# Kernel tuning notes

Measured on AMD Instinct MI355X. Metric: run time of the kernel, lower is better.

## Reference

```python
import jax, jax.numpy as jnp
import numpy as np

def mish(x):
    return x * jnp.tanh(jax.nn.softplus(x))

def setup_inputs() -> dict:
    ANT, RF, DS, G, B = 64, 8, 8, 16, 4096
    BB_DIM = 2 * RF * DS      # 128
    RF_DIM = 2 * ANT * RF     # 1024
    key = jax.random.key(0)
    ks = jax.random.split(key, 10)
    def lin(kw, kb, i, o):
        lim = 1.0 / np.sqrt(i)
        W = jax.random.uniform(kw, (o, i), jnp.float32, -lim, lim)
        b = jax.random.uniform(kb, (o,), jnp.float32, -lim, lim)
        return W, b
    W_rfbb, b_rfbb = lin(ks[0], ks[1], RF_DIM, BB_DIM)
    W_rfrf, b_rfrf = lin(ks[2], ks[3], RF_DIM, RF_DIM)
    W_bbrf, b_bbrf = lin(ks[4], ks[5], BB_DIM, RF_DIM)
    W_bbbb, b_bbbb = lin(ks[6], ks[7], BB_DIM, BB_DIM)
    BB_feature = jax.random.normal(ks[8], (B, G, BB_DIM), jnp.float32)
    RF_feature = jax.random.normal(ks[9], (B, RF_DIM), jnp.float32)
    return {
        "BB_feature": BB_feature, "RF_feature": RF_feature,
        "W_rfbb": W_rfbb, "b_rfbb": b_rfbb,
        "W_rfrf": W_rfrf, "b_rfrf": b_rfrf,
        "W_bbrf": W_bbrf, "b_bbrf": b_bbrf,
        "W_bbbb": W_bbbb, "b_bbbb": b_bbbb,
    }

def reference(BB_feature, RF_feature, W_rfbb, b_rfbb, W_rfrf, b_rfrf, W_bbrf, b_bbrf, W_bbbb, b_bbbb):
    # mean over subcarrier-group dim
    BB_mean = jnp.mean(BB_feature, axis=-2)                      # [B, BB_DIM]
    RF_to_RF = mish(RF_feature @ W_rfrf.T + b_rfrf)              # [B, RF_DIM]
    RF_to_BB = mish(RF_feature @ W_rfbb.T + b_rfbb)              # [B, BB_DIM]
    BB_to_RF = mish(BB_mean @ W_bbrf.T + b_bbrf)                 # [B, RF_DIM]
    BB_to_BB = mish(jnp.einsum('bgi,oi->bgo', BB_feature, W_bbbb) + b_bbbb)  # [B, G, BB_DIM]
    new_RF = RF_to_RF + BB_to_RF
    new_BB = BB_to_BB + RF_to_BB[:, None, :]
    return (new_BB, new_RF)
```

## Files before the change

### kernel.cpp

```cpp
#include <hip/hip_runtime.h>
#include <hip/hip_bf16.h>

typedef __attribute__((ext_vector_type(8))) short short8;
typedef __attribute__((ext_vector_type(4))) short short4v;
typedef __attribute__((ext_vector_type(4))) float floatx4;

#define BDIM 128
#define RDIM 1024
#define NB   4096
#define NG   16

__device__ __forceinline__ float mishf(float x) {
    float e = __expf(x);
    float t = e * (e + 2.0f);
    float r = x * (t / (t + 2.0f));
    return x > 20.0f ? x : r;
}

__device__ __forceinline__ short8 cvt8v(float4 f0, float4 f1) {
    union { __hip_bfloat162 h; unsigned u; } c0, c1, c2, c3;
    c0.h = __float22bfloat162_rn(make_float2(f0.x, f0.y));
    c1.h = __float22bfloat162_rn(make_float2(f0.z, f0.w));
    c2.h = __float22bfloat162_rn(make_float2(f1.x, f1.y));
    c3.h = __float22bfloat162_rn(make_float2(f1.z, f1.w));
    union { short8 s; unsigned u[4]; } r;
    r.u[0] = c0.u; r.u[1] = c1.u; r.u[2] = c2.u; r.u[3] = c3.u;
    return r.s;
}

__device__ __forceinline__ short4v cvt4v(float4 f) {
    union { __hip_bfloat162 h; unsigned u; } c0, c1;
    c0.h = __float22bfloat162_rn(make_float2(f.x, f.y));
    c1.h = __float22bfloat162_rn(make_float2(f.z, f.w));
    union { short4v s; unsigned u[2]; } r;
    r.u[0] = c0.u; r.u[1] = c1.u;
    return r.s;
}

__device__ __forceinline__ void gld16(const void* g, void* l) {
    __builtin_amdgcn_global_load_lds(
        (const __attribute__((address_space(1))) unsigned int*)g,
        (__attribute__((address_space(3))) unsigned int*)l, 16, 0, 0);
}

#define MFMA(a, b, c) __builtin_amdgcn_mfma_f32_16x16x32_bf16(a, b, c, 0, 0, 0)

#define RF_N     4194304u
#define C1       4194304u
#define C2       5242880u
#define C3       5373952u
#define C4       5505024u
#define CT       5521408u

__global__ void __launch_bounds__(256) k_prep(
    const float* __restrict__ bb, const float* __restrict__ rf,
    const float* __restrict__ Wrfrf, const float* __restrict__ Wrfbb,
    const float* __restrict__ Wbbrf, const float* __restrict__ Wbbbb,
    short* __restrict__ bb_b, short* __restrict__ mean_b, short* __restrict__ rf_b,
    short* __restrict__ wrfrf_b, short* __restrict__ wrfbb_b,
    short* __restrict__ wbbrf_b, short* __restrict__ wbbbb_b)
{
    int bid = blockIdx.x;
    int tid = threadIdx.x;
    if (bid < 512) {
        int b = bid * 8 + (tid >> 5);
        int d = (tid & 31) * 4;
        const float4* p = (const float4*)(bb + (size_t)b * (NG * BDIM) + d);
        short* ob = bb_b + (size_t)b * (NG * BDIM) + d;
        float4 s = {0.f, 0.f, 0.f, 0.f};
        #pragma unroll
        for (int g = 0; g < NG; ++g) {
            float4 v = p[g * (BDIM / 4)];
            s.x += v.x; s.y += v.y; s.z += v.z; s.w += v.w;
            *(short4v*)(ob + g * BDIM) = cvt4v(v);
        }
        s.x *= 0.0625f; s.y *= 0.0625f; s.z *= 0.0625f; s.w *= 0.0625f;
        *(short4v*)(mean_b + (size_t)b * BDIM + d) = cvt4v(s);
    } else {
        size_t t = (size_t)(bid - 512) * 256 + tid;
        for (size_t base = t * 8; base < CT; base += (size_t)512 * 256 * 8) {
            const float* s; short* dst; size_t off;
            if (base < C1)      { s = rf;    dst = rf_b;    off = base; }
            else if (base < C2) { s = Wrfrf; dst = wrfrf_b; off = base - C1; }
            else if (base < C3) { s = Wrfbb; dst = wrfbb_b; off = base - C2; }
            else if (base < C4) { s = Wbbrf; dst = wbbrf_b; off = base - C3; }
            else                { s = Wbbbb; dst = wbbbb_b; off = base - C4; }
            float4 f0 = ((const float4*)(s + off))[0];
            float4 f1 = ((const float4*)(s + off))[1];
            *(short8*)(dst + off) = cvt8v(f0, f1);
        }
    }
}

__global__ void __launch_bounds__(256) k_newrf(
    const short* __restrict__ rfb,
    const short* __restrict__ meanb,
    const short* __restrict__ wrfrfb,
    const float* __restrict__ brfrf,
    const short* __restrict__ wbbrfb,
    const float* __restrict__ bbbrf,
    const short* __restrict__ wrfbbb,
    const float* __restrict__ brfbb,
    float* __restrict__ out,
    float* __restrict__ rf2bb)
{
    __shared__ alignas(16) short As[2][128 * 64];
    __shared__ alignas(16) short Bs[2][64 * 64];
    __shared__ alignas(16) short Ws2[2][16 * 64];
    int tid = threadIdx.x;
    int wave = tid >> 6, lane = tid & 63;
    int r = lane & 15, quad = lane >> 4;
    int wm = (wave & 1) * 64, wn = (wave >> 1) * 32;
    int mt = blockIdx.x >> 4, nt = blockIdx.x & 15;
    int m0 = mt * 128, n0 = nt * 64;
    bool doP = (nt < 8);

    int srow = lane >> 3;
    int scol = ((lane & 7) ^ srow) * 8;

    const short* aB = rfb    + (size_t)(m0 + wave * 32 + srow) * RDIM + scol;
    const short* bB = wrfrfb + (size_t)(n0 + wave * 16 + srow) * RDIM + scol;
    const short* wB = wrfbbb + (size_t)(nt * 16 + srow) * RDIM + scol;

    floatx4 acc1[4][2], acc2[4][2], acc3[4];
    #pragma unroll
    for (int mi = 0; mi < 4; ++mi) {
        acc1[mi][0] = floatx4{0.f,0.f,0.f,0.f}; acc1[mi][1] = acc1[mi][0];
        acc2[mi][0] = acc1[mi][0]; acc2[mi][1] = acc1[mi][0];
        acc3[mi] = acc1[mi][0];
    }

    auto stage1 = [&](int buf, int k) {
        #pragma unroll
        for (int j = 0; j < 4; ++j)
            gld16(aB + (size_t)j * 8 * RDIM + k, &As[buf][(wave * 32 + j * 8) * 64]);
        #pragma unroll
        for (int j = 0; j < 2; ++j)
            gld16(bB + (size_t)j * 8 * RDIM + k, &Bs[buf][(wave * 16 + j * 8) * 64]);
        if (doP && wave == 0) {
            #pragma unroll
            for (int j = 0; j < 2; ++j)
                gld16(wB + (size_t)j * 8 * RDIM + k, &Ws2[buf][j * 8 * 64]);
        }
    };

    stage1(0, 0);
    __syncthreads();

    for (int it = 0; it < 16; ++it) {
        int buf = it & 1;
        if (it < 15) stage1(buf ^ 1, (it + 1) * 64);
        const short* Ac = As[buf];
        const short* Bc = Bs[buf];
        const short* Wc = Ws2[buf];
        #pragma unroll
        for (int kk = 0; kk < 2; ++kk) {
            int sw = (((kk << 2) + quad) ^ (r & 7)) << 3;
            short8 af[4];
            #pragma unroll
            for (int mi = 0; mi < 4; ++mi)
                af[mi] = *(const short8*)&Ac[(wm + mi * 16 + r) * 64 + sw];
            short8 bf0 = *(const short8*)&Bc[(wn + r) * 64 + sw];
            short8 bf1 = *(const short8*)&Bc[(wn + 16 + r) * 64 + sw];
            #pragma unroll
            for (int mi = 0; mi < 4; ++mi) {
                acc1[mi][0] = MFMA(af[mi], bf0, acc1[mi][0]);
                acc1[mi][1] = MFMA(af[mi], bf1, acc1[mi][1]);
            }
            if (doP && (wave & 2) == 0) {
                short8 b2 = *(const short8*)&Wc[r * 64 + sw];
                #pragma unroll
                for (int mi = 0; mi < 4; ++mi) acc3[mi] = MFMA(af[mi], b2, acc3[mi]);
            }
        }
        __syncthreads();
    }

    const short* a2B = meanb  + (size_t)(m0 + wave * 32 + srow) * BDIM + scol;
    const short* b2B = wbbrfb + (size_t)(n0 + wave * 16 + srow) * BDIM + scol;
    auto stage2 = [&](int buf, int k) {
        #pragma unroll
        for (int j = 0; j < 4; ++j)
            gld16(a2B + (size_t)j * 8 * BDIM + k, &As[buf][(wave * 32 + j * 8) * 64]);
        #pragma unroll
        for (int j = 0; j < 2; ++j)
            gld16(b2B + (size_t)j * 8 * BDIM + k, &Bs[buf][(wave * 16 + j * 8) * 64]);
    };
    stage2(0, 0);
    __syncthreads();
    for (int it = 0; it < 2; ++it) {
        int buf = it & 1;
        if (it < 1) stage2(1, 64);
        const short* Ac = As[buf];
        const short* Bc = Bs[buf];
        #pragma unroll
        for (int kk = 0; kk < 2; ++kk) {
            int sw = (((kk << 2) + quad) ^ (r & 7)) << 3;
            short8 af[4];
            #pragma unroll
            for (int mi = 0; mi < 4; ++mi)
                af[mi] = *(const short8*)&Ac[(wm + mi * 16 + r) * 64 + sw];
            short8 bf0 = *(const short8*)&Bc[(wn + r) * 64 + sw];
            short8 bf1 = *(const short8*)&Bc[(wn + 16 + r) * 64 + sw];
            #pragma unroll
            for (int mi = 0; mi < 4; ++mi) {
                acc2[mi][0] = MFMA(af[mi], bf0, acc2[mi][0]);
                acc2[mi][1] = MFMA(af[mi], bf1, acc2[mi][1]);
            }
        }
        __syncthreads();
    }

    #pragma unroll
    for (int nj = 0; nj < 2; ++nj) {
        int col = n0 + wn + nj * 16 + r;
        float b1 = brfrf[col];
        float b2 = bbbrf[col];
        #pragma unroll
        for (int mi = 0; mi < 4; ++mi) {
            #pragma unroll
            for (int g = 0; g < 4; ++g) {
                int row = m0 + wm + mi * 16 + quad * 4 + g;
                out[(size_t)row * RDIM + col] =
                    mishf(acc1[mi][nj][g] + b1) + mishf(acc2[mi][nj][g] + b2);
            }
        }
    }
    if (doP && (wave & 2) == 0) {
        int col = nt * 16 + r;
        float bs = brfbb[col];
        #pragma unroll
        for (int mi = 0; mi < 4; ++mi) {
            #pragma unroll
            for (int g = 0; g < 4; ++g) {
                int row = m0 + wm + mi * 16 + quad * 4 + g;
                rf2bb[(size_t)row * BDIM + col] = mishf(acc3[mi][g] + bs);
            }
        }
    }
}

__global__ void __launch_bounds__(256) k_newbb(
    const short* __restrict__ bbb,
    const short* __restrict__ wb,
    const float* __restrict__ bias,
    const float* __restrict__ rf2bb,
    float* __restrict__ out)
{
    __shared__ alignas(16) short At[128 * 128];
    __shared__ alignas(16) short Wt[128 * 128];
    int tid = threadIdx.x;
    int wave = tid >> 6, lane = tid & 63;
    int r = lane & 15, quad = lane >> 4;
    size_t m0 = (size_t)blockIdx.x * 128;

    int lrow = lane >> 4;
    int lslot = lane & 15;
    #pragma unroll
    for (int j = 0; j < 8; ++j) {
        int row = wave * 32 + j * 4 + lrow;
        int col = ((lslot ^ (row & 7)) << 3);
        gld16(bbb + (m0 + row) * BDIM + col, &At[(wave * 32 + j * 4) * 128]);
        gld16(wb + (size_t)row * BDIM + col,  &Wt[(wave * 32 + j * 4) * 128]);
    }

    floatx4 acc[2][8];
    #pragma unroll
    for (int i = 0; i < 2; ++i)
        #pragma unroll
        for (int j = 0; j < 8; ++j) acc[i][j] = floatx4{0.f,0.f,0.f,0.f};

    __syncthreads();

    #pragma unroll
    for (int kc = 0; kc < 4; ++kc) {
        int sw = (((kc << 2) + quad) ^ (r & 7)) << 3;
        short8 a0 = *(const short8*)&At[(wave * 32 + r) * 128 + sw];
        short8 a1 = *(const short8*)&At[(wave * 32 + 16 + r) * 128 + sw];
        #pragma unroll
        for (int nj = 0; nj < 8; ++nj) {
            short8 b = *(const short8*)&Wt[(nj * 16 + r) * 128 + sw];
            acc[0][nj] = MFMA(a0, b, acc[0][nj]);
            acc[1][nj] = MFMA(a1, b, acc[1][nj]);
        }
    }

    #pragma unroll
    for (int mi = 0; mi < 2; ++mi) {
        #pragma unroll
        for (int nj = 0; nj < 8; ++nj) {
            int col = nj * 16 + r;
            float bs = bias[col];
            #pragma unroll
            for (int g = 0; g < 4; ++g) {
                size_t row = m0 + wave * 32 + mi * 16 + quad * 4 + g;
                out[row * BDIM + col] = mishf(acc[mi][nj][g] + bs) + rf2bb[(row >> 4) * BDIM + col];
            }
        }
    }
}

extern "C" void kernel_launch(void* const* d_in, const int* in_sizes, int n_in,
                              void* d_out, int out_size, void* d_ws, size_t ws_size,
                              hipStream_t stream) {
    const float* BB    = (const float*)d_in[0];
    const float* RF    = (const float*)d_in[1];
    const float* Wrfbb = (const float*)d_in[2];
    const float* brfbb = (const float*)d_in[3];
    const float* Wrfrf = (const float*)d_in[4];
    const float* brfrf = (const float*)d_in[5];
    const float* Wbbrf = (const float*)d_in[6];
    const float* bbbrf = (const float*)d_in[7];
    const float* Wbbbb = (const float*)d_in[8];
    const float* bbbbb = (const float*)d_in[9];

    float* outBB = (float*)d_out;
    float* outRF = outBB + (size_t)NB * NG * BDIM;

    char* w = (char*)d_ws;
    short* mean_b  = (short*)(w);
    short* rf_b    = (short*)(w + 1048576);
    short* wrfrf_b = (short*)(w + 9437184);
    short* wrfbb_b = (short*)(w + 11534336);
    short* wbbrf_b = (short*)(w + 11796480);
    short* wbbbb_b = (short*)(w + 12058624);
    short* bb_b    = (short*)(w + 12091392);
    float* rf2bb   = (float*)(w + 28868608);

    k_prep <<<1024, 256, 0, stream>>>(BB, RF, Wrfrf, Wrfbb, Wbbrf, Wbbbb,
                                      bb_b, mean_b, rf_b, wrfrf_b, wrfbb_b,
                                      wbbrf_b, wbbbb_b);
    k_newrf<<<512, 256, 0, stream>>>(rf_b, mean_b, wrfrf_b, brfrf, wbbrf_b, bbbrf,
                                     wrfbb_b, brfbb, outRF, rf2bb);
    k_newbb<<<512, 256, 0, stream>>>(bb_b, wbbbb_b, bbbbb, rf2bb, outBB);
}
```

Before: 153.0 us.

## Split RF-to-BB GEMM into separate blocks and use register-staged LDS loads

```diff
diff --git a/kernel.cpp b/kernel.cpp
--- a/kernel.cpp
+++ b/kernel.cpp
@@ -9,6 +9,7 @@
 #define RDIM 1024
 #define NB   4096
 #define NG   16
+#define LDP  66
 
 __device__ __forceinline__ float mishf(float x) {
     float e = __expf(x);
@@ -45,12 +46,12 @@
 
 #define MFMA(a, b, c) __builtin_amdgcn_mfma_f32_16x16x32_bf16(a, b, c, 0, 0, 0)
 
-#define RF_N     4194304u
 #define C1       4194304u
 #define C2       5242880u
 #define C3       5373952u
 #define C4       5505024u
 #define CT       5521408u
+#define FLATB    1536
 
 __global__ void __launch_bounds__(256) k_prep(
     const float* __restrict__ bb, const float* __restrict__ rf,
@@ -78,7 +79,7 @@
         *(short4v*)(mean_b + (size_t)b * BDIM + d) = cvt4v(s);
     } else {
         size_t t = (size_t)(bid - 512) * 256 + tid;
-        for (size_t base = t * 8; base < CT; base += (size_t)512 * 256 * 8) {
+        for (size_t base = t * 8; base < CT; base += (size_t)FLATB * 256 * 8) {
             const float* s; short* dst; size_t off;
             if (base < C1)      { s = rf;    dst = rf_b;    off = base; }
             else if (base < C2) { s = Wrfrf; dst = wrfrf_b; off = base - C1; }
@@ -104,137 +105,125 @@
     float* __restrict__ out,
     float* __restrict__ rf2bb)
 {
-    __shared__ alignas(16) short As[2][128 * 64];
-    __shared__ alignas(16) short Bs[2][64 * 64];
-    __shared__ alignas(16) short Ws2[2][16 * 64];
+    __shared__ alignas(16) short As[2][128 * LDP];
+    __shared__ alignas(16) short Bs[2][64 * LDP];
     int tid = threadIdx.x;
     int wave = tid >> 6, lane = tid & 63;
     int r = lane & 15, quad = lane >> 4;
     int wm = (wave & 1) * 64, wn = (wave >> 1) * 32;
-    int mt = blockIdx.x >> 4, nt = blockIdx.x & 15;
-    int m0 = mt * 128, n0 = nt * 64;
-    bool doP = (nt < 8);
-
-    int srow = lane >> 3;
-    int scol = ((lane & 7) ^ srow) * 8;
-
-    const short* aB = rfb    + (size_t)(m0 + wave * 32 + srow) * RDIM + scol;
-    const short* bB = wrfrfb + (size_t)(n0 + wave * 16 + srow) * RDIM + scol;
-    const short* wB = wrfbbb + (size_t)(nt * 16 + srow) * RDIM + scol;
-
-    floatx4 acc1[4][2], acc2[4][2], acc3[4];
+    int bid = blockIdx.x;
+    int nt = bid % 18, mt = bid / 18;
+    int m0 = mt * 128;
+    bool isP = (nt >= 16);
+    const short* Bsrc = isP ? (wrfbbb + (size_t)(nt - 16) * 64 * RDIM)
+                            : (wrfrfb + (size_t)nt * 64 * RDIM);
+
+    int srow = tid >> 3;
+    int sslot = tid & 7;
+    int wsl = ((sslot ^ (srow & 7)) << 3);
+    int soff = srow * LDP + wsl;
+
+    const short* aG = rfb + (size_t)(m0 + srow) * RDIM + sslot * 8;
+    const short* bG = Bsrc + (size_t)srow * RDIM + sslot * 8;
+
+    floatx4 acc1[4][2], acc2[4][2];
     #pragma unroll
     for (int mi = 0; mi < 4; ++mi) {
         acc1[mi][0] = floatx4{0.f,0.f,0.f,0.f}; acc1[mi][1] = acc1[mi][0];
         acc2[mi][0] = acc1[mi][0]; acc2[mi][1] = acc1[mi][0];
-        acc3[mi] = acc1[mi][0];
-    }
-
-    auto stage1 = [&](int buf, int k) {
-        #pragma unroll
-        for (int j = 0; j < 4; ++j)
-            gld16(aB + (size_t)j * 8 * RDIM + k, &As[buf][(wave * 32 + j * 8) * 64]);
-        #pragma unroll
-        for (int j = 0; j < 2; ++j)
-            gld16(bB + (size_t)j * 8 * RDIM + k, &Bs[buf][(wave * 16 + j * 8) * 64]);
-        if (doP && wave == 0) {
-            #pragma unroll
-            for (int j = 0; j < 2; ++j)
-                gld16(wB + (size_t)j * 8 * RDIM + k, &Ws2[buf][j * 8 * 64]);
-        }
+    }
+
+    short8 ar[4], br[2];
+    auto gload = [&](int k) {
+        #pragma unroll
+        for (int j = 0; j < 4; ++j) ar[j] = *(const short8*)(aG + (size_t)j * 32 * RDIM + k);
+        #pragma unroll
+        for (int j = 0; j < 2; ++j) br[j] = *(const short8*)(bG + (size_t)j * 32 * RDIM + k);
     };
-
-    stage1(0, 0);
-    __syncthreads();
-
-    for (int it = 0; it < 16; ++it) {
-        int buf = it & 1;
-        if (it < 15) stage1(buf ^ 1, (it + 1) * 64);
-        const short* Ac = As[buf];
-        const short* Bc = Bs[buf];
-        const short* Wc = Ws2[buf];
+    auto lwrite = [&](int buf) {
+        #pragma unroll
+        for (int j = 0; j < 4; ++j) *(short8*)&As[buf][j * 32 * LDP + soff] = ar[j];
+        #pragma unroll
+        for (int j = 0; j < 2; ++j) *(short8*)&Bs[buf][j * 32 * LDP + soff] = br[j];
+    };
+    auto compute_tile = [&](const short* Ac, const short* Bc, floatx4 (&acc)[4][2]) {
         #pragma unroll
         for (int kk = 0; kk < 2; ++kk) {
             int sw = (((kk << 2) + quad) ^ (r & 7)) << 3;
             short8 af[4];
             #pragma unroll
             for (int mi = 0; mi < 4; ++mi)
-                af[mi] = *(const short8*)&Ac[(wm + mi * 16 + r) * 64 + sw];
-            short8 bf0 = *(const short8*)&Bc[(wn + r) * 64 + sw];
-            short8 bf1 = *(const short8*)&Bc[(wn + 16 + r) * 64 + sw];
+                af[mi] = *(const short8*)&Ac[(wm + mi * 16 + r) * LDP + sw];
+            short8 bf0 = *(const short8*)&Bc[(wn + r) * LDP + sw];
+            short8 bf1 = *(const short8*)&Bc[(wn + 16 + r) * LDP + sw];
             #pragma unroll
             for (int mi = 0; mi < 4; ++mi) {
-                acc1[mi][0] = MFMA(af[mi], bf0, acc1[mi][0]);
-                acc1[mi][1] = MFMA(af[mi], bf1, acc1[mi][1]);
+                acc[mi][0] = MFMA(af[mi], bf0, acc[mi][0]);
+                acc[mi][1] = MFMA(af[mi], bf1, acc[mi][1]);
             }
-            if (doP && (wave & 2) == 0) {
-                short8 b2 = *(const short8*)&Wc[r * 64 + sw];
+        }
+    };
+
+    gload(0);
+    lwrite(0);
+    gload(64);
+    __syncthreads();
+
+    for (int it = 0; it < 16; ++it) {
+        int buf = it & 1;
+        compute_tile(As[buf], Bs[buf], acc1);
+        if (it < 15) lwrite(buf ^ 1);
+        if (it < 14) gload((it + 2) * 64);
+        __syncthreads();
+    }
+
+    if (!isP) {
+        const short* a2G = meanb  + (size_t)(m0 + srow) * BDIM + sslot * 8;
+        const short* b2G = wbbrfb + (size_t)(nt * 64 + srow) * BDIM + sslot * 8;
+        #pragma unroll
+        for (int j = 0; j < 4; ++j) ar[j] = *(const short8*)(a2G + (size_t)j * 32 * BDIM);
+        #pragma unroll
+        for (int j = 0; j < 2; ++j) br[j] = *(const short8*)(b2G + (size_t)j * 32 * BDIM);
+        lwrite(0);
+        #pragma unroll
+        for (int j = 0; j < 4; ++j) ar[j] = *(const short8*)(a2G + (size_t)j * 32 * BDIM + 64);
+        #pragma unroll
+        for (int j = 0; j < 2; ++j) br[j] = *(const short8*)(b2G + (size_t)j * 32 * BDIM + 64);
+        __syncthreads();
+        compute_tile(As[0], Bs[0], acc2);
+        lwrite(1);
+        __syncthreads();
+        compute_tile(As[1], Bs[1], acc2);
+    }
+
+    if (!isP) {
+        #pragma unroll
+        for (int nj = 0; nj < 2; ++nj) {
+            int col = nt * 64 + wn + nj * 16 + r;
+            float b1 = brfrf[col];
+            float b2 = bbbrf[col];
+            #pragma unroll
+            for (int mi = 0; mi < 4; ++mi) {
                 #pragma unroll
-                for (int mi = 0; mi < 4; ++mi) acc3[mi] = MFMA(af[mi], b2, acc3[mi]);
+                for (int g = 0; g < 4; ++g) {
+                    int row = m0 + wm + mi * 16 + quad * 4 + g;
+                    out[(size_t)row * RDIM + col] =
+                        mishf(acc1[mi][nj][g] + b1) + mishf(acc2[mi][nj][g] + b2);
+                }
             }
         }
-        __syncthreads();
-    }
-
-    const short* a2B = meanb  + (size_t)(m0 + wave * 32 + srow) * BDIM + scol;
-    const short* b2B = wbbrfb + (size_t)(n0 + wave * 16 + srow) * BDIM + scol;
-    auto stage2 = [&](int buf, int k) {
-        #pragma unroll
-        for (int j = 0; j < 4; ++j)
-            gld16(a2B + (size_t)j * 8 * BDIM + k, &As[buf][(wave * 32 + j * 8) * 64]);
-        #pragma unroll
-        for (int j = 0; j < 2; ++j)
-            gld16(b2B + (size_t)j * 8 * BDIM + k, &Bs[buf][(wave * 16 + j * 8) * 64]);
-    };
-    stage2(0, 0);
-    __syncthreads();
-    for (int it = 0; it < 2; ++it) {
-        int buf = it & 1;
-        if (it < 1) stage2(1, 64);
-        const short* Ac = As[buf];
-        const short* Bc = Bs[buf];
-        #pragma unroll
-        for (int kk = 0; kk < 2; ++kk) {
-            int sw = (((kk << 2) + quad) ^ (r & 7)) << 3;
-            short8 af[4];
-            #pragma unroll
-            for (int mi = 0; mi < 4; ++mi)
-                af[mi] = *(const short8*)&Ac[(wm + mi * 16 + r) * 64 + sw];
-            short8 bf0 = *(const short8*)&Bc[(wn + r) * 64 + sw];
-            short8 bf1 = *(const short8*)&Bc[(wn + 16 + r) * 64 + sw];
+    } else {
+        #pragma unroll
+        for (int nj = 0; nj < 2; ++nj) {
+            int colL = (nt - 16) * 64 + wn + nj * 16 + r;
+            float bs = brfbb[colL];
             #pragma unroll
             for (int mi = 0; mi < 4; ++mi) {
-                acc2[mi][0] = MFMA(af[mi], bf0, acc2[mi][0]);
-                acc2[mi][1] = MFMA(af[mi], bf1, acc2[mi][1]);
-            }
-        }
-        __syncthreads();
-    }
-
-    #pragma unroll
-    for (int nj = 0; nj < 2; ++nj) {
-        int col = n0 + wn + nj * 16 + r;
-        float b1 = brfrf[col];
-        float b2 = bbbrf[col];
-        #pragma unroll
-        for (int mi = 0; mi < 4; ++mi) {
-            #pragma unroll
-            for (int g = 0; g < 4; ++g) {
-                int row = m0 + wm + mi * 16 + quad * 4 + g;
-                out[(size_t)row * RDIM + col] =
-                    mishf(acc1[mi][nj][g] + b1) + mishf(acc2[mi][nj][g] + b2);
-            }
-        }
-    }
-    if (doP && (wave & 2) == 0) {
-        int col = nt * 16 + r;
-        float bs = brfbb[col];
-        #pragma unroll
-        for (int mi = 0; mi < 4; ++mi) {
-            #pragma unroll
-            for (int g = 0; g < 4; ++g) {
-                int row = m0 + wm + mi * 16 + quad * 4 + g;
-                rf2bb[(size_t)row * BDIM + col] = mishf(acc3[mi][g] + bs);
+                #pragma unroll
+                for (int g = 0; g < 4; ++g) {
+                    int row = m0 + wm + mi * 16 + quad * 4 + g;
+                    rf2bb[(size_t)row * BDIM + colL] = mishf(acc1[mi][nj][g] + bs);
+                }
             }
         }
     }
@@ -247,7 +236,6 @@
     const float* __restrict__ rf2bb,
     float* __restrict__ out)
 {
-    __shared__ alignas(16) short At[128 * 128];
     __shared__ alignas(16) short Wt[128 * 128];
     int tid = threadIdx.x;
     int wave = tid >> 6, lane = tid & 63;
@@ -260,9 +248,16 @@
     for (int j = 0; j < 8; ++j) {
         int row = wave * 32 + j * 4 + lrow;
         int col = ((lslot ^ (row & 7)) << 3);
-        gld16(bbb + (m0 + row) * BDIM + col, &At[(wave * 32 + j * 4) * 128]);
-        gld16(wb + (size_t)row * BDIM + col,  &Wt[(wave * 32 + j * 4) * 128]);
-    }
+        gld16(wb + (size_t)row * BDIM + col, &Wt[(wave * 32 + j * 4) * 128]);
+    }
+
+    const short* aB = bbb + (m0 + wave * 32 + r) * BDIM + quad * 8;
+    short8 afr[2][4];
+    #pragma unroll
+    for (int mi = 0; mi < 2; ++mi)
+        #pragma unroll
+        for (int kc = 0; kc < 4; ++kc)
+            afr[mi][kc] = *(const short8*)(aB + mi * 16 * BDIM + kc * 32);
 
     floatx4 acc[2][8];
     #pragma unroll
@@ -275,13 +270,11 @@
     #pragma unroll
     for (int kc = 0; kc < 4; ++kc) {
         int sw = (((kc << 2) + quad) ^ (r & 7)) << 3;
-        short8 a0 = *(const short8*)&At[(wave * 32 + r) * 128 + sw];
-        short8 a1 = *(const short8*)&At[(wave * 32 + 16 + r) * 128 + sw];
         #pragma unroll
         for (int nj = 0; nj < 8; ++nj) {
             short8 b = *(const short8*)&Wt[(nj * 16 + r) * 128 + sw];
-            acc[0][nj] = MFMA(a0, b, acc[0][nj]);
-            acc[1][nj] = MFMA(a1, b, acc[1][nj]);
+            acc[0][nj] = MFMA(afr[0][kc], b, acc[0][nj]);
+            acc[1][nj] = MFMA(afr[1][kc], b, acc[1][nj]);
         }
     }
 
@@ -327,10 +320,10 @@
     short* bb_b    = (short*)(w + 12091392);
     float* rf2bb   = (float*)(w + 28868608);
 
-    k_prep <<<1024, 256, 0, stream>>>(BB, RF, Wrfrf, Wrfbb, Wbbrf, Wbbbb,
-                                      bb_b, mean_b, rf_b, wrfrf_b, wrfbb_b,
-                                      wbbrf_b, wbbbb_b);
-    k_newrf<<<512, 256, 0, stream>>>(rf_b, mean_b, wrfrf_b, brfrf, wbbrf_b, bbbrf,
+    k_prep <<<512 + FLATB, 256, 0, stream>>>(BB, RF, Wrfrf, Wrfbb, Wbbrf, Wbbbb,
+                                             bb_b, mean_b, rf_b, wrfrf_b, wrfbb_b,
+                                             wbbrf_b, wbbbb_b);
+    k_newrf<<<576, 256, 0, stream>>>(rf_b, mean_b, wrfrf_b, brfrf, wbbrf_b, bbbrf,
                                      wrfbb_b, brfbb, outRF, rf2bb);
     k_newbb<<<512, 256, 0, stream>>>(bb_b, wbbbb_b, bbbbb, rf2bb, outBB);
 }
```

New measurement: 210.9 us. +37.8%, slower.
